# Performance work log

Hardware: AMD Instinct MI355X
Metric: run time of the kernel (lower is better)

Reference implementation:

```python
import jax, jax.numpy as jnp
import numpy as np

V, E, H, B, P, Q = 100000, 300, 256, 64, 400, 50
NEG = -1e7


def _gru_param(k, s=0.08):
    k1, k2, k3, k4 = jax.random.split(k, 4)
    return (jax.random.normal(k1, (2, 3 * H, E)) * s,
            jax.random.normal(k2, (2, 3 * H, H)) * s,
            jax.random.normal(k3, (2, 3 * H)) * s,
            jax.random.normal(k4, (2, 3 * H)) * s)


def setup_inputs() -> dict:
    key = jax.random.key(0)
    ks = jax.random.split(key, 10)
    emb = (jax.random.normal(ks[0], (V, E)) * 0.1).at[0].set(0.0)  # padding_idx=0 row zeroed
    passage = jax.random.randint(ks[1], (B, P), 1, V)
    question = jax.random.randint(ks[2], (B, Q), 1, V)
    # variable lengths, padding (token 0) at the tail like pack_padded_sequence assumes
    p_len = 200 + (jnp.arange(B) * 7) % (P - 200)
    q_len = 20 + (jnp.arange(B) * 3) % (Q - 20)
    passage = jnp.where(jnp.arange(P)[None, :] < p_len[:, None], passage, 0)
    question = jnp.where(jnp.arange(Q)[None, :] < q_len[:, None], question, 0)
    pW_ih, pW_hh, pb_ih, pb_hh = _gru_param(ks[3])
    qW_ih, qW_hh, qb_ih, qb_hh = _gru_param(ks[4])
    start_w = jax.random.normal(ks[5], (6 * H,)) * 0.05
    start_b = jax.random.normal(ks[6], ()) * 0.05
    end_w = jax.random.normal(ks[7], (6 * H,)) * 0.05
    end_b = jax.random.normal(ks[8], ()) * 0.05
    return dict(passage=passage, question=question, emb=emb,
                pW_ih=pW_ih, pW_hh=pW_hh, pb_ih=pb_ih, pb_hh=pb_hh,
                qW_ih=qW_ih, qW_hh=qW_hh, qb_ih=qb_ih, qb_hh=qb_hh,
                start_w=start_w, start_b=start_b, end_w=end_w, end_b=end_b)


def bi_gru(x, mask, Wih, Whh, bih, bhh):
    """Bidirectional GRU with packed-sequence-equivalent masking.
    x: (B,T,E), mask: (B,T) float. Returns (B,T,2H). Padded outputs are 0,
    and the backward pass starts at the true last token (mask freezes state)."""
    m = mask[..., None]                                          # (B,T,1)
    xproj = jnp.einsum('bte,dhe->dbth', x, Wih) + bih[:, None, None, :]  # (2,B,T,3H)

    def run(xp, mm, Whh_d, bhh_d):
        def step(h, inp):
            xt, mt = inp                                         # (B,3H),(B,1)
            hp = h @ Whh_d.T + bhh_d
            r = jax.nn.sigmoid(xt[:, :H] + hp[:, :H])
            z = jax.nn.sigmoid(xt[:, H:2 * H] + hp[:, H:2 * H])
            n = jnp.tanh(xt[:, 2 * H:] + r * hp[:, 2 * H:])
            h_new = (1 - z) * n + z * h
            h_new = mt * h_new + (1 - mt) * h
            return h_new, h_new * mt
        h0 = jnp.zeros((xp.shape[0], H), xp.dtype)
        _, out = jax.lax.scan(step, h0, (xp.transpose(1, 0, 2), mm.transpose(1, 0, 2)))
        return out.transpose(1, 0, 2)                            # (B,T,H)

    fwd = run(xproj[0], m, Whh[0], bhh[0])
    bwd = run(xproj[1][:, ::-1], m[:, ::-1], Whh[1], bhh[1])[:, ::-1]
    return jnp.concatenate([fwd, bwd], axis=-1)


def reference(passage, question, emb,
              pW_ih, pW_hh, pb_ih, pb_hh,
              qW_ih, qW_hh, qb_ih, qb_hh,
              start_w, start_b, end_w, end_b):
    p_mask = (passage != 0).astype(jnp.float32)                  # (B,P)
    q_mask = (question != 0).astype(jnp.float32)                 # (B,Q)
    Hp = bi_gru(emb[passage], p_mask, pW_ih, pW_hh, pb_ih, pb_hh)  # (B,P,2H)
    Hq = bi_gru(emb[question], q_mask, qW_ih, qW_hh, qb_ih, qb_hh)  # (B,Q,2H)

    # Trilinear attention: decompose Linear over the cat([p, q, p*q]) terms
    w1, w2, w3 = start_w[:2 * H], start_w[2 * H:4 * H], start_w[4 * H:]
    scores = (Hp @ w1)[:, :, None] + (Hq @ w2)[:, None, :] \
        + jnp.einsum('bpd,bqd->bpq', Hp * w3, Hq) + start_b      # (B,P,Q)

    # allennlp masked_softmax: softmax(vector*mask) * mask, renormalized
    a = jax.nn.softmax(scores * q_mask[:, None, :], axis=-1) * q_mask[:, None, :]
    a = a / (a.sum(axis=-1, keepdims=True) + 1e-13)

    wavg = jnp.einsum('bpq,bqd->bpd', a, Hq)                     # (B,P,2H)
    combined = jnp.concatenate([Hp, wavg, Hp * wavg], axis=-1)   # (B,P,6H)

    start_logits = jnp.where(p_mask > 0, combined @ start_w + start_b, NEG)
    end_logits = jnp.where(p_mask > 0, combined @ end_w + end_b, NEG)
    log_mask = jnp.log(p_mask + 1e-45)
    softmax_start = jax.nn.log_softmax(start_logits + log_mask, axis=-1)
    softmax_end = jax.nn.log_softmax(end_logits + log_mask, axis=-1)
    return start_logits, end_logits, softmax_start, softmax_end
```

## Files before the change

### kernel.cpp

```cpp
#include <hip/hip_runtime.h>
#include <math.h>

constexpr int Bb = 64;
constexpr int Pp = 400;
constexpr int Qq = 50;
constexpr int Ee = 300;
constexpr int Hh = 256;
constexpr int H3 = 768;
constexpr int Dd = 512;

#define NEGC (-10000000.0f)
#define LOGTINY (-103.278929903f)

typedef _Float16 h2 __attribute__((ext_vector_type(2)));
typedef _Float16 f16x8 __attribute__((ext_vector_type(8)));
typedef float f32x4 __attribute__((ext_vector_type(4)));

__device__ __forceinline__ float allred(float v){
  #pragma unroll
  for (int off = 1; off < 64; off <<= 1) v += __shfl_xor(v, off);
  return v;
}
__device__ __forceinline__ float allmax(float v){
  #pragma unroll
  for (int off = 1; off < 64; off <<= 1) v = fmaxf(v, __shfl_xor(v, off));
  return v;
}
__device__ __forceinline__ float sigm(float x){ return 1.f / (1.f + expf(-x)); }

__device__ __forceinline__ float dot2f(unsigned a, unsigned b, float c){
#if __has_builtin(__builtin_amdgcn_fdot2)
  return __builtin_amdgcn_fdot2(__builtin_bit_cast(h2, a), __builtin_bit_cast(h2, b), c, false);
#else
  float r = c;
  asm("v_dot2_f32_f16 %0, %1, %2, %0" : "+v"(r) : "v"(a), "v"(b));
  return r;
#endif
}

#define U4C(v,c) ((c)==0?(v).x:((c)==1?(v).y:((c)==2?(v).z:(v).w)))

__global__ __launch_bounds__(256) void gather_a(const int* __restrict__ ptok,
                                                const int* __restrict__ qtok,
                                                const float* __restrict__ emb,
                                                _Float16* __restrict__ Agp,
                                                _Float16* __restrict__ Agq){
  int idx = blockIdx.x * 256 + threadIdx.x;
  if (idx >= (25600 + 3200) * 40) return;
  int ck = idx % 40;
  int row = idx / 40;
  int tokv; _Float16* dst;
  if (row < 25600){ tokv = ptok[row]; dst = Agp + (size_t)row * 320; }
  else { int r = row - 25600; tokv = qtok[r]; dst = Agq + (size_t)r * 320; }
  int c = ck * 8;
  const float* src = emb + (size_t)tokv * Ee;
  f16x8 v;
  #pragma unroll
  for (int i = 0; i < 8; ++i) v[i] = (c + i < Ee) ? (_Float16)src[c + i] : (_Float16)0.f;
  *(f16x8*)(dst + c) = v;
}

__global__ __launch_bounds__(256) void prep_wih16(const float* __restrict__ pW,
                                                  const float* __restrict__ qW,
                                                  _Float16* __restrict__ wih16){
  int idx = blockIdx.x * 256 + threadIdx.x;
  if (idx >= 2 * 2 * 768 * 160) return;
  int col2 = idx % 160;
  int r = idx / 160;
  int g = r / 1536;
  int dh = r % 1536;
  int c = col2 * 2;
  const float* W = g ? qW : pW;
  float2 v = make_float2(0.f, 0.f);
  if (c < Ee) v = *(const float2*)(W + (size_t)dh * Ee + c);
  h2 o = { (_Float16)v.x, (_Float16)v.y };
  *(h2*)(wih16 + (size_t)r * 320 + c) = o;
}

__global__ __launch_bounds__(256) void prep_w16(const float* __restrict__ pW,
                                                const float* __restrict__ qW,
                                                unsigned* __restrict__ w16){
  int idx = blockIdx.x * 256 + threadIdx.x;
  if (idx >= 2 * 2 * 3 * 16 * 512 * 4) return;
  int c = idx & 3;
  int t = (idx >> 2) & 511;
  int q = (idx >> 11) & 15;
  int gg = idx >> 15;
  int gate = gg % 3, gd = gg / 3;
  int d = gd & 1, g = gd >> 1;
  int j = t & 255, half = t >> 8;
  int p = half * 64 + q * 4 + c;
  int row = gate * 256 + j;
  const float* W = g ? qW : pW;
  const float* src = W + ((size_t)d * H3 + row) * Hh + 2 * p;
  _Float16 a = (_Float16)src[0], b = (_Float16)src[1];
  unsigned short ua, ub;
  __builtin_memcpy(&ua, &a, 2); __builtin_memcpy(&ub, &b, 2);
  unsigned val = (unsigned)ua | ((unsigned)ub << 16);

  size_t u4idx;
  if (q < 5)       u4idx = ((size_t)gg * 5 + q) * 512 + t;
  else if (q < 11) u4idx = 30720 + ((size_t)gg * 6 + (q - 5)) * 512 + t;
  else             u4idx = 67584 + ((size_t)gg * 5 + (q - 11)) * 512 + t;
  w16[u4idx * 4 + c] = val;
}

__global__ __launch_bounds__(512) void xproj_mfma(const _Float16* __restrict__ Ag,
                                                  const _Float16* __restrict__ wih16,
                                                  const float* __restrict__ bih,
                                                  _Float16* __restrict__ xp, int T){
  __shared__ __align__(16) _Float16 Af[128][72];
  __shared__ __align__(16) _Float16 Bf[128][72];
  int tid = threadIdx.x;
  int m0 = blockIdx.y * 128;
  int nt = blockIdx.x;
  int d = nt / 6, h0 = (nt % 6) * 128;
  int wid = tid >> 6, lane = tid & 63;
  int wr = wid >> 2, wc = wid & 3;

  int r0 = tid >> 3;
  int r1 = (tid + 512) >> 3;
  int cc = (tid & 7) * 8;
  const _Float16* eA0 = Ag + (size_t)(m0 + r0) * 320;
  const _Float16* eA1 = Ag + (size_t)(m0 + r1) * 320;
  const _Float16* wB0 = wih16 + ((size_t)d * H3 + h0 + r0) * 320;
  const _Float16* wB1 = wih16 + ((size_t)d * H3 + h0 + r1) * 320;

  f32x4 acc[4][2] = {};

  for (int k0 = 0; k0 < 320; k0 += 64){
    *(f16x8*)&Af[r0][cc] = *(const f16x8*)(eA0 + k0 + cc);
    *(f16x8*)&Af[r1][cc] = *(const f16x8*)(eA1 + k0 + cc);
    *(f16x8*)&Bf[r0][cc] = *(const f16x8*)(wB0 + k0 + cc);
    *(f16x8*)&Bf[r1][cc] = *(const f16x8*)(wB1 + k0 + cc);
    __syncthreads();
    #pragma unroll
    for (int kc = 0; kc < 2; ++kc){
      int kb = kc * 32 + (lane >> 4) * 8;
      f16x8 af[4], bf[2];
      #pragma unroll
      for (int i = 0; i < 4; ++i) af[i] = *(const f16x8*)&Af[wr * 64 + i * 16 + (lane & 15)][kb];
      #pragma unroll
      for (int jn = 0; jn < 2; ++jn) bf[jn] = *(const f16x8*)&Bf[wc * 32 + jn * 16 + (lane & 15)][kb];
      #pragma unroll
      for (int i = 0; i < 4; ++i)
        #pragma unroll
        for (int jn = 0; jn < 2; ++jn)
          acc[i][jn] = __builtin_amdgcn_mfma_f32_16x16x32_f16(af[i], bf[jn], acc[i][jn], 0, 0, 0);
    }
    __syncthreads();
  }

  #pragma unroll
  for (int jn = 0; jn < 2; ++jn){
    int h = h0 + wc * 32 + jn * 16 + (lane & 15);
    float bv = bih[d * H3 + h];
    #pragma unroll
    for (int i = 0; i < 4; ++i){
      #pragma unroll
      for (int r = 0; r < 4; ++r){
        int m = m0 + wr * 64 + i * 16 + (lane >> 4) * 4 + r;
        int bI = m / T, tI = m - bI * T;
        xp[(((size_t)d * Bb + bI) * T + tI) * H3 + h] = (_Float16)(acc[i][jn][r] + bv);
      }
    }
  }
}

__global__ __launch_bounds__(512)
void gru_kernel(const int* __restrict__ ptok,
                const int* __restrict__ qtok,
                const _Float16* __restrict__ xpp,
                const _Float16* __restrict__ xpq,
                const unsigned* __restrict__ w16,
                const float* __restrict__ pbhh,
                const float* __restrict__ qbhh,
                float* __restrict__ Hp,
                float* __restrict__ Hq){
  int wg = blockIdx.x;
  bool isp = wg < 128;
  int lw = isp ? wg : wg - 128;
  int d = lw & 1, b = lw >> 1;
  int T = isp ? Pp : Qq;
  const int* tok = (isp ? ptok : qtok) + b * T;
  const _Float16* xrow = (isp ? xpp : xpq) + ((size_t)d * Bb + b) * T * H3;
  int gd = (isp ? 0 : 2) + d;
  const float* bhh = (isp ? pbhh : qbhh) + d * H3;
  float* Hout = (isp ? Hp : Hq) + (size_t)b * T * Dd + d * Hh;

  __shared__ __align__(16) uint4 ldsW[18 * 512];
  __shared__ unsigned hbuf[2][128];
  __shared__ float pa[Hh], pb[Hh], pn[Hh];

  int t = threadIdx.x;
  int j = t & 255, half = t >> 8, lane = t & 63;
  const uint4* u4w = (const uint4*)w16;

  unsigned wr0[20], wr1[20], wr2[20];
  #pragma unroll
  for (int q = 0; q < 5; ++q){
    uint4 v0 = u4w[((size_t)(gd * 3 + 0) * 5 + q) * 512 + t];
    uint4 v1 = u4w[((size_t)(gd * 3 + 1) * 5 + q) * 512 + t];
    uint4 v2 = u4w[((size_t)(gd * 3 + 2) * 5 + q) * 512 + t];
    wr0[4 * q + 0] = v0.x; wr0[4 * q + 1] = v0.y; wr0[4 * q + 2] = v0.z; wr0[4 * q + 3] = v0.w;
    wr1[4 * q + 0] = v1.x; wr1[4 * q + 1] = v1.y; wr1[4 * q + 2] = v1.z; wr1[4 * q + 3] = v1.w;
    wr2[4 * q + 0] = v2.x; wr2[4 * q + 1] = v2.y; wr2[4 * q + 2] = v2.z; wr2[4 * q + 3] = v2.w;
  }
  #pragma unroll
  for (int i = 0; i < 20; ++i){
    asm volatile("" : "+v"(wr0[i]));
    asm volatile("" : "+v"(wr1[i]));
    asm volatile("" : "+v"(wr2[i]));
  }

  #pragma unroll
  for (int u = 0; u < 18; ++u)
    ldsW[u * 512 + t] = u4w[30720 + ((size_t)gd * 18 + u) * 512 + t];
  const uint4* wS = u4w + 67584 + (size_t)(gd * 3) * 5 * 512;

  float bh0 = bhh[j], bh1 = bhh[Hh + j], bh2 = bhh[2 * Hh + j];
  float h_old = 0.f;
  if (t < 128) hbuf[1][t] = 0u;
  __syncthreads();

  int t0 = d ? (T - 1) : 0;
  float pre0 = 0.f, pre1 = 0.f, pre2 = 0.f;
  if (half == 0){
    pre0 = (float)xrow[(size_t)t0 * H3 + j];
    pre1 = (float)xrow[(size_t)t0 * H3 + Hh + j];
    pre2 = (float)xrow[(size_t)t0 * H3 + 2 * Hh + j];
  }

  for (int s = 0; s < T; ++s){
    int tt = d ? (T - 1 - s) : s;
    unsigned vh = hbuf[(s + 1) & 1][half * 64 + lane];
    float a0 = 0.f, a1 = 0.f, a2 = 0.f;

    #define LPH(ql) { \
      uint4 l0 = ldsW[(0 * 6 + (ql)) * 512 + t]; \
      uint4 l1 = ldsW[(1 * 6 + (ql)) * 512 + t]; \
      uint4 l2 = ldsW[(2 * 6 + (ql)) * 512 + t]; \
      _Pragma("unroll") \
      for (int c = 0; c < 4; ++c){ \
        unsigned hv = (unsigned)__builtin_amdgcn_readlane((int)vh, 20 + (ql) * 4 + c); \
        a0 = dot2f(U4C(l0, c), hv, a0); \
        a1 = dot2f(U4C(l1, c), hv, a1); \
        a2 = dot2f(U4C(l2, c), hv, a2); } }
    #define SCQ(ACC, si, A) { _Pragma("unroll") \
      for (int c = 0; c < 4; ++c){ \
        unsigned hv = (unsigned)__builtin_amdgcn_readlane((int)vh, 44 + (si) * 4 + c); \
        ACC = dot2f(U4C(A, c), hv, ACC); } }
    #define SISSG(g, A0, A1, A2, A3, A4) \
      uint4 A0 = wS[((g) * 5 + 0) * 512 + t]; \
      uint4 A1 = wS[((g) * 5 + 1) * 512 + t]; \
      uint4 A2 = wS[((g) * 5 + 2) * 512 + t]; \
      uint4 A3 = wS[((g) * 5 + 3) * 512 + t]; \
      uint4 A4 = wS[((g) * 5 + 4) * 512 + t];

    SISSG(0, s00, s01, s02, s03, s04)

    #pragma unroll
    for (int q = 0; q < 5; ++q)
      #pragma unroll
      for (int c = 0; c < 4; ++c){
        unsigned hv = (unsigned)__builtin_amdgcn_readlane((int)vh, 4 * q + c);
        a0 = dot2f(wr0[q * 4 + c], hv, a0);
        a1 = dot2f(wr1[q * 4 + c], hv, a1);
        a2 = dot2f(wr2[q * 4 + c], hv, a2);
      }

    LPH(0) LPH(1)
    SCQ(a0, 0, s00) SCQ(a0, 1, s01) SCQ(a0, 2, s02) SCQ(a0, 3, s03) SCQ(a0, 4, s04)
    SISSG(1, s10, s11, s12, s13, s14)
    LPH(2) LPH(3)
    SCQ(a1, 0, s10) SCQ(a1, 1, s11) SCQ(a1, 2, s12) SCQ(a1, 3, s13) SCQ(a1, 4, s14)
    SISSG(2, s20, s21, s22, s23, s24)
    LPH(4) LPH(5)
    SCQ(a2, 0, s20) SCQ(a2, 1, s21) SCQ(a2, 2, s22) SCQ(a2, 3, s23) SCQ(a2, 4, s24)
    #undef LPH
    #undef SCQ
    #undef SISSG

    if (half == 1){ pa[j] = a0; pb[j] = a1; pn[j] = a2; }
    __syncthreads();
    if (half == 0){
      float xt0 = pre0, xt1 = pre1, xt2 = pre2;
      if (s + 1 < T){
        int tn = d ? (T - 2 - s) : (s + 1);
        pre0 = (float)xrow[(size_t)tn * H3 + j];
        pre1 = (float)xrow[(size_t)tn * H3 + Hh + j];
        pre2 = (float)xrow[(size_t)tn * H3 + 2 * Hh + j];
      }
      float g0 = a0 + pa[j] + bh0;
      float g1 = a1 + pb[j] + bh1;
      float g2 = a2 + pn[j] + bh2;
      float r = sigm(xt0 + g0);
      float z = sigm(xt1 + g1);
      float n = tanhf(xt2 + r * g2);
      float hnew = (1.f - z) * n + z * h_old;
      float m = (tok[tt] != 0) ? 1.f : 0.f;
      float hm = m * hnew + (1.f - m) * h_old;
      h_old = hm;
      ((_Float16*)hbuf[s & 1])[j] = (_Float16)hm;
      Hout[(size_t)tt * Dd + j] = hm * m;
    }
    __syncthreads();
  }
}

__global__ __launch_bounds__(512) void attn_kernel(const float* __restrict__ Hp,
                                                   const float* __restrict__ Hq,
                                                   const int* __restrict__ ptok,
                                                   const int* __restrict__ qtok,
                                                   const float* __restrict__ start_w,
                                                   const float* __restrict__ sbp,
                                                   const float* __restrict__ end_w,
                                                   const float* __restrict__ ebp,
                                                   float* __restrict__ out){
  extern __shared__ __align__(16) float lds[];
  float* hqs = lds;
  float* s2s = hqs + Qq * Dd;
  float* qms = s2s + 64;
  float* scw = qms + 64;
  float* aw  = scw + 512;

  int b = blockIdx.y, pc = blockIdx.x;
  int tid = threadIdx.x, wid = tid >> 6, lane = tid & 63;
  float sb = sbp[0], eb = ebp[0];

  float w1r[8], w2r[8], w3r[8], e1r[8], e2r[8], e3r[8];
  #pragma unroll
  for (int i = 0; i < 8; ++i){
    int c = lane * 8 + i;
    w1r[i] = start_w[c]; w2r[i] = start_w[Dd + c]; w3r[i] = start_w[2 * Dd + c];
    e1r[i] = end_w[c];   e2r[i] = end_w[Dd + c];   e3r[i] = end_w[2 * Dd + c];
  }
  for (int idx = tid; idx < Qq * Dd; idx += 512) hqs[idx] = Hq[(size_t)b * Qq * Dd + idx];
  __syncthreads();

  for (int q = wid; q < Qq; q += 8){
    float part = 0.f;
    const float* hq = hqs + q * Dd + lane * 8;
    #pragma unroll
    for (int i = 0; i < 8; ++i) part += hq[i] * w2r[i];
    part = allred(part);
    if (lane == 0){
      s2s[q] = part;
      qms[q] = (qtok[b * Qq + q] != 0) ? 1.f : 0.f;
    }
  }
  __syncthreads();

  for (int p = pc * 100 + wid; p < pc * 100 + 100; p += 8){
    const float* hprow = Hp + ((size_t)b * Pp + p) * Dd + lane * 8;
    float4 hv0 = *(const float4*)hprow;
    float4 hv1 = *(const float4*)(hprow + 4);
    float hpc[8] = {hv0.x, hv0.y, hv0.z, hv0.w, hv1.x, hv1.y, hv1.z, hv1.w};
    float hw3[8], he3[8];
    float s1 = 0.f, ed = 0.f;
    #pragma unroll
    for (int i = 0; i < 8; ++i){
      hw3[i] = hpc[i] * w3r[i];
      he3[i] = hpc[i] * e3r[i];
      s1 += hpc[i] * w1r[i];
      ed += hpc[i] * e1r[i];
    }
    #pragma unroll
    for (int off = 1; off < 64; off <<= 1){
      s1 += __shfl_xor(s1, off);
      ed += __shfl_xor(ed, off);
    }
    for (int q = 0; q < Qq; ++q){
      const float4* hq4 = (const float4*)(hqs + q * Dd + lane * 8);
      float4 a0 = hq4[0], a1 = hq4[1];
      float dot = hw3[0] * a0.x + hw3[1] * a0.y + hw3[2] * a0.z + hw3[3] * a0.w
                + hw3[4] * a1.x + hw3[5] * a1.y + hw3[6] * a1.z + hw3[7] * a1.w;
      dot = allred(dot);
      if (lane == 0) scw[wid * 64 + q] = (s1 + s2s[q] + dot + sb) * qms[q];
    }
    float v = (lane < Qq) ? scw[wid * 64 + lane] : -1e30f;
    float M = allmax(v);
    float ev = (lane < Qq) ? expf(v - M) : 0.f;
    float S = allred(ev);
    float am = (lane < Qq) ? (ev / S) * qms[lane] : 0.f;
    float Sm = allred(am);
    float af = am / (Sm + 1e-13f);
    if (lane < Qq) aw[wid * 64 + lane] = af;
    float wv[8] = {0.f, 0.f, 0.f, 0.f, 0.f, 0.f, 0.f, 0.f};
    for (int q = 0; q < Qq; ++q){
      float aq = aw[wid * 64 + q];
      const float4* hq4 = (const float4*)(hqs + q * Dd + lane * 8);
      float4 a0 = hq4[0], a1 = hq4[1];
      wv[0] += aq * a0.x; wv[1] += aq * a0.y; wv[2] += aq * a0.z; wv[3] += aq * a0.w;
      wv[4] += aq * a1.x; wv[5] += aq * a1.y; wv[6] += aq * a1.z; wv[7] += aq * a1.w;
    }
    float acc2 = 0.f, acc3 = 0.f, acc4 = 0.f, acc5 = 0.f;
    #pragma unroll
    for (int i = 0; i < 8; ++i){
      acc2 += wv[i] * w2r[i];
      acc3 += hw3[i] * wv[i];
      acc4 += wv[i] * e2r[i];
      acc5 += he3[i] * wv[i];
    }
    #pragma unroll
    for (int off = 1; off < 64; off <<= 1){
      acc2 += __shfl_xor(acc2, off);
      acc3 += __shfl_xor(acc3, off);
      acc4 += __shfl_xor(acc4, off);
      acc5 += __shfl_xor(acc5, off);
    }
    if (lane == 0){
      bool pm = (ptok[b * Pp + p] != 0);
      out[(size_t)b * Pp + p]                   = pm ? (s1 + acc2 + acc3 + sb) : NEGC;
      out[(size_t)Bb * Pp + (size_t)b * Pp + p] = pm ? (ed + acc4 + acc5 + eb) : NEGC;
    }
  }
}

__global__ __launch_bounds__(512) void lsm_kernel(const int* __restrict__ ptok,
                                                  float* __restrict__ out){
  int b = blockIdx.x >> 1, sel = blockIdx.x & 1;
  const float* lg = out + (size_t)sel * Bb * Pp + (size_t)b * Pp;
  float* o = out + (size_t)(2 + sel) * Bb * Pp + (size_t)b * Pp;
  int tid = threadIdx.x;
  __shared__ float red1[8];
  __shared__ float red2[8];
  float x = -1e30f;
  if (tid < Pp) x = lg[tid] + ((ptok[b * Pp + tid] != 0) ? 0.f : LOGTINY);
  float m = allmax(x);
  if ((tid & 63) == 0) red1[tid >> 6] = m;
  __syncthreads();
  float M = red1[0];
  #pragma unroll
  for (int i = 1; i < 8; ++i) M = fmaxf(M, red1[i]);
  float e = (tid < Pp) ? expf(x - M) : 0.f;
  float s = allred(e);
  if ((tid & 63) == 0) red2[tid >> 6] = s;
  __syncthreads();
  float S = 0.f;
  #pragma unroll
  for (int i = 0; i < 8; ++i) S += red2[i];
  if (tid < Pp) o[tid] = (x - M) - logf(S);
}

extern "C" void kernel_launch(void* const* d_in, const int* in_sizes, int n_in,
                              void* d_out, int out_size, void* d_ws, size_t ws_size,
                              hipStream_t stream){
  const int*   passage  = (const int*)d_in[0];
  const int*   question = (const int*)d_in[1];
  const float* emb      = (const float*)d_in[2];
  const float* pW_ih    = (const float*)d_in[3];
  const float* pW_hh    = (const float*)d_in[4];
  const float* pb_ih    = (const float*)d_in[5];
  const float* pb_hh    = (const float*)d_in[6];
  const float* qW_ih    = (const float*)d_in[7];
  const float* qW_hh    = (const float*)d_in[8];
  const float* qb_ih    = (const float*)d_in[9];
  const float* qb_hh    = (const float*)d_in[10];
  const float* start_w  = (const float*)d_in[11];
  const float* start_b  = (const float*)d_in[12];
  const float* end_w    = (const float*)d_in[13];
  const float* end_b    = (const float*)d_in[14];
  float* out = (float*)d_out;

  float*     ws    = (float*)d_ws;
  unsigned*  w16   = (unsigned*)ws;
  _Float16*  wih16 = (_Float16*)(ws + 393216);
  _Float16*  Agp   = (_Float16*)(ws + 884736);
  _Float16*  Agq   = (_Float16*)(ws + 4980736);
  _Float16*  xpp   = (_Float16*)(ws + 5492736);
  _Float16*  xpq   = (_Float16*)(ws + 25153536);
  float*     Hp    = ws + 27611136;
  float*     Hq    = ws + 40718336;

  hipLaunchKernelGGL(prep_w16, dim3(1536), dim3(256), 0, stream, pW_hh, qW_hh, w16);
  hipLaunchKernelGGL(gather_a, dim3(4500), dim3(256), 0, stream,
                     passage, question, emb, Agp, Agq);
  hipLaunchKernelGGL(prep_wih16, dim3(1920), dim3(256), 0, stream, pW_ih, qW_ih, wih16);
  hipLaunchKernelGGL(xproj_mfma, dim3(12, 200), dim3(512), 0, stream,
                     Agp, wih16, pb_ih, xpp, Pp);
  hipLaunchKernelGGL(xproj_mfma, dim3(12, 25), dim3(512), 0, stream,
                     Agq, wih16 + (size_t)2 * H3 * 320, qb_ih, xpq, Qq);
  hipLaunchKernelGGL(gru_kernel, dim3(256), dim3(512), 0, stream,
                     passage, question, xpp, xpq, w16, pb_hh, qb_hh, Hp, Hq);
  size_t attn_lds = (size_t)(Qq * Dd + 64 + 64 + 512 + 512) * sizeof(float);
  hipLaunchKernelGGL(attn_kernel, dim3(4, 64), dim3(512), attn_lds, stream,
                     Hp, Hq, passage, question, start_w, start_b, end_w, end_b, out);
  hipLaunchKernelGGL(lsm_kernel, dim3(128), dim3(512), 0, stream, passage, out);
}
```

Measured before the change: 964.9 us.

## Split GRU recurrent matvec across four K-quarters with 1024-thread blocks

The recurrent GRU kernel now splits the hidden-state reduction into four quarters instead of two, launching 1024 threads per block. Weights are repacked into a new register/LDS/global streaming layout so each thread holds 28 register words, 9 LDS uint4 chunks and 8 streamed chunks. Three partial sums per gate are reduced through shared memory. This shortens each thread's serial dot-product chain on the latency-bound time loop, at the cost of more threads, a larger cross-wave reduction and possible register pressure under the 1024 launch bound.

```diff
diff --git a/kernel.cpp b/kernel.cpp
--- a/kernel.cpp
+++ b/kernel.cpp
@@ -81,28 +81,34 @@
                                                 const float* __restrict__ qW,
                                                 unsigned* __restrict__ w16){
   int idx = blockIdx.x * 256 + threadIdx.x;
-  if (idx >= 2 * 2 * 3 * 16 * 512 * 4) return;
+  if (idx >= 393216) return;
   int c = idx & 3;
-  int t = (idx >> 2) & 511;
-  int q = (idx >> 11) & 15;
-  int gg = idx >> 15;
-  int gate = gg % 3, gd = gg / 3;
-  int d = gd & 1, g = gd >> 1;
-  int j = t & 255, half = t >> 8;
-  int p = half * 64 + q * 4 + c;
-  int row = gate * 256 + j;
-  const float* W = g ? qW : pW;
+  int t = (idx >> 2) & 1023;
+  int B = idx >> 12;
+  int gd, g, ql;
+  if (B < 28){
+    gd = B / 7; int rb = B % 7;
+    ql = rb / 3; g = rb % 3;
+  } else if (B < 64){
+    int lb0 = B - 28; gd = lb0 / 9; int lb = lb0 % 9;
+    if (lb < 2){ ql = 2; g = lb + 1; }
+    else if (lb < 8){ int v = lb - 2; ql = 3 + v / 3; g = v % 3; }
+    else { ql = 5; g = 0; }
+  } else {
+    int sb0 = B - 64; gd = sb0 / 8; int sb = sb0 % 8;
+    if (sb < 2){ ql = 5; g = sb + 1; }
+    else { int v = sb - 2; ql = 6 + v / 3; g = v % 3; }
+  }
+  int j = t & 255, qq = t >> 8;
+  int p = qq * 32 + ql * 4 + c;
+  int row = g * 256 + j;
+  int d = gd & 1, kind = gd >> 1;
+  const float* W = kind ? qW : pW;
   const float* src = W + ((size_t)d * H3 + row) * Hh + 2 * p;
-  _Float16 a = (_Float16)src[0], b = (_Float16)src[1];
+  _Float16 a = (_Float16)src[0], bb = (_Float16)src[1];
   unsigned short ua, ub;
-  __builtin_memcpy(&ua, &a, 2); __builtin_memcpy(&ub, &b, 2);
-  unsigned val = (unsigned)ua | ((unsigned)ub << 16);
-
-  size_t u4idx;
-  if (q < 5)       u4idx = ((size_t)gg * 5 + q) * 512 + t;
-  else if (q < 11) u4idx = 30720 + ((size_t)gg * 6 + (q - 5)) * 512 + t;
-  else             u4idx = 67584 + ((size_t)gg * 5 + (q - 11)) * 512 + t;
-  w16[u4idx * 4 + c] = val;
+  __builtin_memcpy(&ua, &a, 2); __builtin_memcpy(&ub, &bb, 2);
+  w16[idx] = (unsigned)ua | ((unsigned)ub << 16);
 }
 
 __global__ __launch_bounds__(512) void xproj_mfma(const _Float16* __restrict__ Ag,
@@ -167,7 +173,7 @@
   }
 }
 
-__global__ __launch_bounds__(512)
+__global__ __launch_bounds__(1024)
 void gru_kernel(const int* __restrict__ ptok,
                 const int* __restrict__ qtok,
                 const _Float16* __restrict__ xpp,
@@ -188,35 +194,27 @@
   const float* bhh = (isp ? pbhh : qbhh) + d * H3;
   float* Hout = (isp ? Hp : Hq) + (size_t)b * T * Dd + d * Hh;
 
-  __shared__ __align__(16) uint4 ldsW[18 * 512];
+  __shared__ __align__(16) uint4 ldsW[9 * 1024];
+  __shared__ float part[3][3][Hh];
   __shared__ unsigned hbuf[2][128];
-  __shared__ float pa[Hh], pb[Hh], pn[Hh];
 
   int t = threadIdx.x;
-  int j = t & 255, half = t >> 8, lane = t & 63;
+  int j = t & 255, qq = t >> 8, lane = t & 63;
   const uint4* u4w = (const uint4*)w16;
 
-  unsigned wr0[20], wr1[20], wr2[20];
-  #pragma unroll
-  for (int q = 0; q < 5; ++q){
-    uint4 v0 = u4w[((size_t)(gd * 3 + 0) * 5 + q) * 512 + t];
-    uint4 v1 = u4w[((size_t)(gd * 3 + 1) * 5 + q) * 512 + t];
-    uint4 v2 = u4w[((size_t)(gd * 3 + 2) * 5 + q) * 512 + t];
-    wr0[4 * q + 0] = v0.x; wr0[4 * q + 1] = v0.y; wr0[4 * q + 2] = v0.z; wr0[4 * q + 3] = v0.w;
-    wr1[4 * q + 0] = v1.x; wr1[4 * q + 1] = v1.y; wr1[4 * q + 2] = v1.z; wr1[4 * q + 3] = v1.w;
-    wr2[4 * q + 0] = v2.x; wr2[4 * q + 1] = v2.y; wr2[4 * q + 2] = v2.z; wr2[4 * q + 3] = v2.w;
-  }
-  #pragma unroll
-  for (int i = 0; i < 20; ++i){
-    asm volatile("" : "+v"(wr0[i]));
-    asm volatile("" : "+v"(wr1[i]));
-    asm volatile("" : "+v"(wr2[i]));
-  }
-
-  #pragma unroll
-  for (int u = 0; u < 18; ++u)
-    ldsW[u * 512 + t] = u4w[30720 + ((size_t)gd * 18 + u) * 512 + t];
-  const uint4* wS = u4w + 67584 + (size_t)(gd * 3) * 5 * 512;
+  unsigned wrR[28];
+  #pragma unroll
+  for (int rb = 0; rb < 7; ++rb){
+    uint4 v = u4w[((size_t)gd * 7 + rb) * 1024 + t];
+    wrR[4 * rb + 0] = v.x; wrR[4 * rb + 1] = v.y; wrR[4 * rb + 2] = v.z; wrR[4 * rb + 3] = v.w;
+  }
+  #pragma unroll
+  for (int i = 0; i < 28; ++i) asm volatile("" : "+v"(wrR[i]));
+
+  #pragma unroll
+  for (int lb = 0; lb < 9; ++lb)
+    ldsW[lb * 1024 + t] = u4w[28 * 1024 + ((size_t)gd * 9 + lb) * 1024 + t];
+  const uint4* wS = u4w + 64 * 1024 + (size_t)gd * 8 * 1024;
 
   float bh0 = bhh[j], bh1 = bhh[Hh + j], bh2 = bhh[2 * Hh + j];
   float h_old = 0.f;
@@ -225,7 +223,7 @@
 
   int t0 = d ? (T - 1) : 0;
   float pre0 = 0.f, pre1 = 0.f, pre2 = 0.f;
-  if (half == 0){
+  if (qq == 0){
     pre0 = (float)xrow[(size_t)t0 * H3 + j];
     pre1 = (float)xrow[(size_t)t0 * H3 + Hh + j];
     pre2 = (float)xrow[(size_t)t0 * H3 + 2 * Hh + j];
@@ -233,57 +231,95 @@
 
   for (int s = 0; s < T; ++s){
     int tt = d ? (T - 1 - s) : s;
-    unsigned vh = hbuf[(s + 1) & 1][half * 64 + lane];
+    unsigned vh = hbuf[(s + 1) & 1][qq * 32 + (lane & 31)];
     float a0 = 0.f, a1 = 0.f, a2 = 0.f;
 
-    #define LPH(ql) { \
-      uint4 l0 = ldsW[(0 * 6 + (ql)) * 512 + t]; \
-      uint4 l1 = ldsW[(1 * 6 + (ql)) * 512 + t]; \
-      uint4 l2 = ldsW[(2 * 6 + (ql)) * 512 + t]; \
-      _Pragma("unroll") \
-      for (int c = 0; c < 4; ++c){ \
-        unsigned hv = (unsigned)__builtin_amdgcn_readlane((int)vh, 20 + (ql) * 4 + c); \
-        a0 = dot2f(U4C(l0, c), hv, a0); \
-        a1 = dot2f(U4C(l1, c), hv, a1); \
-        a2 = dot2f(U4C(l2, c), hv, a2); } }
-    #define SCQ(ACC, si, A) { _Pragma("unroll") \
-      for (int c = 0; c < 4; ++c){ \
-        unsigned hv = (unsigned)__builtin_amdgcn_readlane((int)vh, 44 + (si) * 4 + c); \
-        ACC = dot2f(U4C(A, c), hv, ACC); } }
-    #define SISSG(g, A0, A1, A2, A3, A4) \
-      uint4 A0 = wS[((g) * 5 + 0) * 512 + t]; \
-      uint4 A1 = wS[((g) * 5 + 1) * 512 + t]; \
-      uint4 A2 = wS[((g) * 5 + 2) * 512 + t]; \
-      uint4 A3 = wS[((g) * 5 + 3) * 512 + t]; \
-      uint4 A4 = wS[((g) * 5 + 4) * 512 + t];
-
-    SISSG(0, s00, s01, s02, s03, s04)
-
-    #pragma unroll
-    for (int q = 0; q < 5; ++q)
+    uint4 sA0 = wS[0 * 1024 + t], sA1 = wS[1 * 1024 + t];
+
+    #pragma unroll
+    for (int c = 0; c < 4; ++c){
+      unsigned hv = (unsigned)__builtin_amdgcn_readlane((int)vh, c);
+      a0 = dot2f(wrR[0 + c], hv, a0);
+      a1 = dot2f(wrR[4 + c], hv, a1);
+      a2 = dot2f(wrR[8 + c], hv, a2);
+    }
+    #pragma unroll
+    for (int c = 0; c < 4; ++c){
+      unsigned hv = (unsigned)__builtin_amdgcn_readlane((int)vh, 4 + c);
+      a0 = dot2f(wrR[12 + c], hv, a0);
+      a1 = dot2f(wrR[16 + c], hv, a1);
+      a2 = dot2f(wrR[20 + c], hv, a2);
+    }
+    #pragma unroll
+    for (int c = 0; c < 4; ++c){
+      unsigned hv = (unsigned)__builtin_amdgcn_readlane((int)vh, 8 + c);
+      a0 = dot2f(wrR[24 + c], hv, a0);
+    }
+
+    uint4 sB0 = wS[2 * 1024 + t], sB1 = wS[3 * 1024 + t], sB2 = wS[4 * 1024 + t];
+
+    { uint4 l1 = ldsW[0 * 1024 + t], l2 = ldsW[1 * 1024 + t];
       #pragma unroll
       for (int c = 0; c < 4; ++c){
-        unsigned hv = (unsigned)__builtin_amdgcn_readlane((int)vh, 4 * q + c);
-        a0 = dot2f(wr0[q * 4 + c], hv, a0);
-        a1 = dot2f(wr1[q * 4 + c], hv, a1);
-        a2 = dot2f(wr2[q * 4 + c], hv, a2);
-      }
-
-    LPH(0) LPH(1)
-    SCQ(a0, 0, s00) SCQ(a0, 1, s01) SCQ(a0, 2, s02) SCQ(a0, 3, s03) SCQ(a0, 4, s04)
-    SISSG(1, s10, s11, s12, s13, s14)
-    LPH(2) LPH(3)
-    SCQ(a1, 0, s10) SCQ(a1, 1, s11) SCQ(a1, 2, s12) SCQ(a1, 3, s13) SCQ(a1, 4, s14)
-    SISSG(2, s20, s21, s22, s23, s24)
-    LPH(4) LPH(5)
-    SCQ(a2, 0, s20) SCQ(a2, 1, s21) SCQ(a2, 2, s22) SCQ(a2, 3, s23) SCQ(a2, 4, s24)
-    #undef LPH
-    #undef SCQ
-    #undef SISSG
-
-    if (half == 1){ pa[j] = a0; pb[j] = a1; pn[j] = a2; }
+        unsigned hv = (unsigned)__builtin_amdgcn_readlane((int)vh, 8 + c);
+        a1 = dot2f(U4C(l1, c), hv, a1);
+        a2 = dot2f(U4C(l2, c), hv, a2);
+      } }
+    { uint4 l0 = ldsW[2 * 1024 + t], l1 = ldsW[3 * 1024 + t], l2 = ldsW[4 * 1024 + t];
+      #pragma unroll
+      for (int c = 0; c < 4; ++c){
+        unsigned hv = (unsigned)__builtin_amdgcn_readlane((int)vh, 12 + c);
+        a0 = dot2f(U4C(l0, c), hv, a0);
+        a1 = dot2f(U4C(l1, c), hv, a1);
+        a2 = dot2f(U4C(l2, c), hv, a2);
+      } }
+
+    #pragma unroll
+    for (int c = 0; c < 4; ++c){
+      unsigned hv = (unsigned)__builtin_amdgcn_readlane((int)vh, 20 + c);
+      a1 = dot2f(U4C(sA0, c), hv, a1);
+      a2 = dot2f(U4C(sA1, c), hv, a2);
+    }
+
+    uint4 sC0 = wS[5 * 1024 + t], sC1 = wS[6 * 1024 + t], sC2 = wS[7 * 1024 + t];
+
+    { uint4 l0 = ldsW[5 * 1024 + t], l1 = ldsW[6 * 1024 + t], l2 = ldsW[7 * 1024 + t];
+      #pragma unroll
+      for (int c = 0; c < 4; ++c){
+        unsigned hv = (unsigned)__builtin_amdgcn_readlane((int)vh, 16 + c);
+        a0 = dot2f(U4C(l0, c), hv, a0);
+        a1 = dot2f(U4C(l1, c), hv, a1);
+        a2 = dot2f(U4C(l2, c), hv, a2);
+      } }
+    { uint4 l0 = ldsW[8 * 1024 + t];
+      #pragma unroll
+      for (int c = 0; c < 4; ++c){
+        unsigned hv = (unsigned)__builtin_amdgcn_readlane((int)vh, 20 + c);
+        a0 = dot2f(U4C(l0, c), hv, a0);
+      } }
+
+    #pragma unroll
+    for (int c = 0; c < 4; ++c){
+      unsigned hv = (unsigned)__builtin_amdgcn_readlane((int)vh, 24 + c);
+      a0 = dot2f(U4C(sB0, c), hv, a0);
+      a1 = dot2f(U4C(sB1, c), hv, a1);
+      a2 = dot2f(U4C(sB2, c), hv, a2);
+    }
+    #pragma unroll
+    for (int c = 0; c < 4; ++c){
+      unsigned hv = (unsigned)__builtin_amdgcn_readlane((int)vh, 28 + c);
+      a0 = dot2f(U4C(sC0, c), hv, a0);
+      a1 = dot2f(U4C(sC1, c), hv, a1);
+      a2 = dot2f(U4C(sC2, c), hv, a2);
+    }
+
+    if (qq != 0){
+      part[qq - 1][0][j] = a0;
+      part[qq - 1][1][j] = a1;
+      part[qq - 1][2][j] = a2;
+    }
     __syncthreads();
-    if (half == 0){
+    if (qq == 0){
       float xt0 = pre0, xt1 = pre1, xt2 = pre2;
       if (s + 1 < T){
         int tn = d ? (T - 2 - s) : (s + 1);
@@ -291,9 +327,9 @@
         pre1 = (float)xrow[(size_t)tn * H3 + Hh + j];
         pre2 = (float)xrow[(size_t)tn * H3 + 2 * Hh + j];
       }
-      float g0 = a0 + pa[j] + bh0;
-      float g1 = a1 + pb[j] + bh1;
-      float g2 = a2 + pn[j] + bh2;
+      float g0 = a0 + part[0][0][j] + part[1][0][j] + part[2][0][j] + bh0;
+      float g1 = a1 + part[0][1][j] + part[1][1][j] + part[2][1][j] + bh1;
+      float g2 = a2 + part[0][2][j] + part[1][2][j] + part[2][2][j] + bh2;
       float r = sigm(xt0 + g0);
       float z = sigm(xt1 + g1);
       float n = tanhf(xt2 + r * g2);
@@ -481,7 +517,7 @@
                      Agp, wih16, pb_ih, xpp, Pp);
   hipLaunchKernelGGL(xproj_mfma, dim3(12, 25), dim3(512), 0, stream,
                      Agq, wih16 + (size_t)2 * H3 * 320, qb_ih, xpq, Qq);
-  hipLaunchKernelGGL(gru_kernel, dim3(256), dim3(512), 0, stream,
+  hipLaunchKernelGGL(gru_kernel, dim3(256), dim3(1024), 0, stream,
                      passage, question, xpp, xpq, w16, pb_hh, qb_hh, Hp, Hq);
   size_t attn_lds = (size_t)(Qq * Dd + 64 + 64 + 512 + 512) * sizeof(float);
   hipLaunchKernelGGL(attn_kernel, dim3(4, 64), dim3(512), attn_lds, stream,
```

Measured after the change: 938.9 us. 1.03x faster.
